# Kernel tuning notes

Measured on AMD Instinct MI355X. Metric: run time of the kernel, lower is better.

Reference implementation:

```python
import jax, jax.numpy as jnp
import numpy as np
from functools import partial

HID = 256
HOR = 5

def _lin(k, i, o):
    return jax.random.normal(k, (i, o), jnp.float32) / np.sqrt(i)

def setup_inputs() -> dict:
    key = jax.random.key(0)
    ks = jax.random.split(key, 32)
    B, T, D, Hf, Wf = 4, 16, 768, 16, 16
    H, W = 1024, 1024
    inp = {}
    inp['features'] = jax.random.normal(ks[0], (B, T, D, Hf, Wf), jnp.float32)
    inp['predictions'] = jax.random.uniform(ks[1], (B, T, 1, H, W), dtype=jnp.float32)
    # position encoder: 4 -> HID -> HID
    inp['pe_w1'] = _lin(ks[2], 4, HID); inp['pe_b1'] = jnp.zeros((HID,), jnp.float32)
    inp['pe_w2'] = _lin(ks[3], HID, HID); inp['pe_b2'] = jnp.zeros((HID,), jnp.float32)
    # 2-layer LSTM, gate order i,f,g,o (torch convention)
    inp['wih0'] = _lin(ks[4], HID, 4 * HID); inp['whh0'] = _lin(ks[5], HID, 4 * HID)
    inp['bih0'] = jnp.zeros((4 * HID,), jnp.float32); inp['bhh0'] = jnp.zeros((4 * HID,), jnp.float32)
    inp['wih1'] = _lin(ks[6], HID, 4 * HID); inp['whh1'] = _lin(ks[7], HID, 4 * HID)
    inp['bih1'] = jnp.zeros((4 * HID,), jnp.float32); inp['bhh1'] = jnp.zeros((4 * HID,), jnp.float32)
    # motion predictor: HID -> HID -> HID/2 -> HOR*4
    inp['mp_w1'] = _lin(ks[8], HID, HID); inp['mp_b1'] = jnp.zeros((HID,), jnp.float32)
    inp['mp_w2'] = _lin(ks[9], HID, HID // 2); inp['mp_b2'] = jnp.zeros((HID // 2,), jnp.float32)
    inp['mp_w3'] = _lin(ks[10], HID // 2, HOR * 4); inp['mp_b3'] = jnp.zeros((HOR * 4,), jnp.float32)
    # confidence: HID -> HID/2 -> HOR
    inp['cf_w1'] = _lin(ks[11], HID, HID // 2); inp['cf_b1'] = jnp.zeros((HID // 2,), jnp.float32)
    inp['cf_w2'] = _lin(ks[12], HID // 2, HOR); inp['cf_b2'] = jnp.zeros((HOR,), jnp.float32)
    return inp

def _extract_bboxes(predictions):
    # predictions: (B,T,1,H,W) -> bboxes (B,T,4) in (cx,cy,w,h), normalized
    B, T, _, H, W = predictions.shape
    mask = predictions[:, :, 0] > 0.5  # (B,T,H,W)
    xs = jnp.arange(W, dtype=jnp.float32)           # (W,)
    ys = jnp.arange(H, dtype=jnp.float32)[:, None]  # (H,1)
    big = jnp.float32(H + W)
    x_min = jnp.min(jnp.where(mask, xs, big), axis=(-2, -1))
    x_max = jnp.max(jnp.where(mask, xs, -1.0), axis=(-2, -1))
    y_min = jnp.min(jnp.where(mask, ys, big), axis=(-2, -1))
    y_max = jnp.max(jnp.where(mask, ys, -1.0), axis=(-2, -1))
    has = jnp.any(mask, axis=(-2, -1))  # (B,T)
    cx = (x_min + x_max) / 2.0 / W
    cy = (y_min + y_max) / 2.0 / H
    w = (x_max - x_min) / W
    h = (y_max - y_min) / H
    bbox = jnp.stack([cx, cy, w, h], axis=-1)  # (B,T,4)
    default = jnp.array([0.5, 0.5, 0.1, 0.1], dtype=jnp.float32)
    return jnp.where(has[..., None], bbox, default)

def _lstm_layer(x, wih, whh, bih, bhh):
    # x: (B,T,HID); returns (hs (B,T,H), h_final (B,H))
    B = x.shape[0]
    xg = jnp.einsum('bti,ig->btg', x, wih) + bih  # (B,T,4H)
    def step(carry, xg_t):
        h, c = carry
        g = xg_t + h @ whh + bhh
        i, f, gg, o = jnp.split(g, 4, axis=-1)
        i = jax.nn.sigmoid(i); f = jax.nn.sigmoid(f)
        gg = jnp.tanh(gg); o = jax.nn.sigmoid(o)
        c = f * c + i * gg
        h = o * jnp.tanh(c)
        return (h, c), h
    z = jnp.zeros((B, HID), x.dtype)
    (h, c), hs = jax.lax.scan(step, (z, z), xg.swapaxes(0, 1))
    return hs.swapaxes(0, 1), h

def reference(features, predictions, pe_w1, pe_b1, pe_w2, pe_b2,
              wih0, whh0, bih0, bhh0, wih1, whh1, bih1, bhh1,
              mp_w1, mp_b1, mp_w2, mp_b2, mp_w3, mp_b3,
              cf_w1, cf_b1, cf_w2, cf_b2):
    B, T = features.shape[:2]
    bboxes = _extract_bboxes(predictions)  # (B,T,4)
    pos = jax.nn.relu(bboxes @ pe_w1 + pe_b1)
    pos = jax.nn.relu(pos @ pe_w2 + pe_b2)  # (B,T,HID)
    h1, _ = _lstm_layer(pos, wih0, whh0, bih0, bhh0)
    motion_features, last_hidden = _lstm_layer(h1, wih1, whh1, bih1, bhh1)
    x = jax.nn.relu(last_hidden @ mp_w1 + mp_b1)
    x = jax.nn.relu(x @ mp_w2 + mp_b2)
    predicted_deltas = (x @ mp_w3 + mp_b3).reshape(B, HOR, 4)
    last_bbox = bboxes[:, -1:, :]
    predicted_bboxes = last_bbox + jnp.cumsum(predicted_deltas, axis=1)
    c = jax.nn.relu(last_hidden @ cf_w1 + cf_b1)
    confidence = jax.nn.sigmoid(c @ cf_w2 + cf_b2)  # (B,HOR)
    predicted_locations = predicted_bboxes[..., :2]
    predicted_scales = predicted_bboxes[..., 2:]
    return (predicted_deltas, predicted_bboxes, predicted_locations,
            predicted_scales, motion_features, confidence, bboxes)
```

## Files before the change

kernel.cpp:

```cpp
#include <hip/hip_runtime.h>
#include <math.h>

#define BIGI (1 << 30)

#define PM_OFF    0
#define MM_OFF    8192
#define POS2_OFF  8448
#define HT0_OFF   24832
#define HT2_OFF   57600
#define HT_WORDS  36864

#define OUT_DELTAS 0
#define OUT_PBB    80
#define OUT_LOC    160
#define OUT_SCL    200
#define OUT_MF     240
#define OUT_CONF   16624
#define OUT_BBOX   16644

__device__ __forceinline__ float sigmoidf_(float x) { return 1.0f / (1.0f + expf(-x)); }

__device__ __forceinline__ void storeh(unsigned long long* p, float h, int tag) {
    unsigned long long v =
        ((unsigned long long)(unsigned)tag << 32) | (unsigned long long)__float_as_uint(h);
    __hip_atomic_store(p, v, __ATOMIC_RELAXED, __HIP_MEMORY_SCOPE_AGENT);
}
__device__ __forceinline__ float pollh(const unsigned long long* p, int tag) {
    unsigned long long v = __hip_atomic_load(p, __ATOMIC_RELAXED, __HIP_MEMORY_SCOPE_AGENT);
    while ((int)(v >> 32) != tag) {
        __builtin_amdgcn_s_sleep(1);
        v = __hip_atomic_load(p, __ATOMIC_RELAXED, __HIP_MEMORY_SCOPE_AGENT);
    }
    return __uint_as_float((unsigned)v);
}

__global__ __launch_bounds__(256) void k_minmax(const float4* __restrict__ pred,
                                                int* __restrict__ pm) {
    int img = blockIdx.x >> 5;
    int chunk = blockIdx.x & 31;
    int tid = threadIdx.x;
    int base = img * 262144 + chunk * 8192 + tid;
    int xmn = BIGI, xmx = -1, ymn = BIGI, ymx = -1;
#pragma unroll 4
    for (int i = 0; i < 32; ++i) {
        int idx4 = base + i * 256;
        float4 v = pred[idx4];
        int x = (idx4 << 2) & 1023;
        int y = (idx4 >> 8) & 1023;
        bool m0 = v.x > 0.5f, m1 = v.y > 0.5f, m2 = v.z > 0.5f, m3 = v.w > 0.5f;
        int cmn = m0 ? x : (m1 ? x + 1 : (m2 ? x + 2 : (m3 ? x + 3 : BIGI)));
        int cmx = m3 ? x + 3 : (m2 ? x + 2 : (m1 ? x + 1 : (m0 ? x : -1)));
        xmn = min(xmn, cmn);
        xmx = max(xmx, cmx);
        if (m0 | m1 | m2 | m3) { ymn = min(ymn, y); ymx = max(ymx, y); }
    }
    for (int off = 32; off > 0; off >>= 1) {
        xmn = min(xmn, __shfl_down(xmn, off));
        xmx = max(xmx, __shfl_down(xmx, off));
        ymn = min(ymn, __shfl_down(ymn, off));
        ymx = max(ymx, __shfl_down(ymx, off));
    }
    __shared__ int red[4][4];
    int wave = tid >> 6;
    if ((tid & 63) == 0) { red[0][wave] = xmn; red[1][wave] = xmx; red[2][wave] = ymn; red[3][wave] = ymx; }
    __syncthreads();
    if (tid == 0) {
        xmn = min(min(red[0][0], red[0][1]), min(red[0][2], red[0][3]));
        xmx = max(max(red[1][0], red[1][1]), max(red[1][2], red[1][3]));
        ymn = min(min(red[2][0], red[2][1]), min(red[2][2], red[2][3]));
        ymx = max(max(red[3][0], red[3][1]), max(red[3][2], red[3][3]));
        ((int4*)pm)[blockIdx.x] = make_int4(xmn, xmx, ymn, ymx);
    }
}

__global__ __launch_bounds__(256) void k_prep(const int* __restrict__ pm,
    int* __restrict__ mm, int* __restrict__ ht,
    const float* __restrict__ pe_w1, const float* __restrict__ pe_b1,
    const float* __restrict__ pe_w2, const float* __restrict__ pe_b2,
    float* __restrict__ pos2, float* __restrict__ out) {
    __shared__ float bb[4];
    __shared__ float p1[256];
    int w = blockIdx.x, tid = threadIdx.x;
    for (int i = w * 256 + tid; i < HT_WORDS; i += 64 * 256) ht[i] = 0;
    if (tid < 64) {
        int xmn = BIGI, xmx = -1, ymn = BIGI, ymx = -1;
        if (tid < 32) {
            int4 v = ((const int4*)pm)[w * 32 + tid];
            xmn = v.x; xmx = v.y; ymn = v.z; ymx = v.w;
        }
        for (int off = 32; off > 0; off >>= 1) {
            xmn = min(xmn, __shfl_down(xmn, off));
            xmx = max(xmx, __shfl_down(xmx, off));
            ymn = min(ymn, __shfl_down(ymn, off));
            ymx = max(ymx, __shfl_down(ymx, off));
        }
        if (tid == 0) {
            mm[w * 4 + 0] = xmn; mm[w * 4 + 1] = xmx;
            mm[w * 4 + 2] = ymn; mm[w * 4 + 3] = ymx;
            float cx, cy, bw, bh;
            if (xmx >= 0) {
                cx = (float)(xmn + xmx) * (0.5f / 1024.0f);
                cy = (float)(ymn + ymx) * (0.5f / 1024.0f);
                bw = (float)(xmx - xmn) * (1.0f / 1024.0f);
                bh = (float)(ymx - ymn) * (1.0f / 1024.0f);
            } else { cx = 0.5f; cy = 0.5f; bw = 0.1f; bh = 0.1f; }
            bb[0] = cx; bb[1] = cy; bb[2] = bw; bb[3] = bh;
            out[OUT_BBOX + w * 4 + 0] = cx; out[OUT_BBOX + w * 4 + 1] = cy;
            out[OUT_BBOX + w * 4 + 2] = bw; out[OUT_BBOX + w * 4 + 3] = bh;
        }
    }
    __syncthreads();
    {
        float v = bb[0] * pe_w1[tid] + bb[1] * pe_w1[256 + tid] +
                  bb[2] * pe_w1[512 + tid] + bb[3] * pe_w1[768 + tid] + pe_b1[tid];
        p1[tid] = fmaxf(v, 0.0f);
    }
    __syncthreads();
    float acc = pe_b2[tid];
#pragma unroll 4
    for (int k = 0; k < 256; ++k) acc += p1[k] * pe_w2[k * 256 + tid];
    pos2[w * 256 + tid] = fmaxf(acc, 0.0f);
}

__global__ __launch_bounds__(256, 1) void k_lstm(
    const float* __restrict__ wih0, const float* __restrict__ whh0,
    const float* __restrict__ bih0, const float* __restrict__ bhh0,
    const float* __restrict__ wih1, const float* __restrict__ whh1,
    const float* __restrict__ bih1, const float* __restrict__ bhh1,
    const float* __restrict__ mp_w1, const float* __restrict__ mp_b1,
    const float* __restrict__ mp_w2, const float* __restrict__ mp_b2,
    const float* __restrict__ mp_w3, const float* __restrict__ mp_b3,
    const float* __restrict__ cf_w1, const float* __restrict__ cf_b1,
    const float* __restrict__ cf_w2, const float* __restrict__ cf_b2,
    const float* __restrict__ pos2, unsigned long long* __restrict__ hT0,
    unsigned long long* __restrict__ hT2,
    const int* __restrict__ mm, float* __restrict__ out) {
    __shared__ float px[4096];
    __shared__ float partX[4096];
    __shared__ float xgl[2048];
    __shared__ float hsm[256];
    __shared__ float part[256];
    __shared__ float gatesL[128];
    const int tid = threadIdx.x;
    const int b = blockIdx.x >> 3, g = blockIdx.x & 7;
    const int j = tid & 127, kh = tid >> 7;
    const int col = ((j >> 5) << 8) + g * 32 + (j & 31);
    float4 wreg[32];

    for (int layer = 0; layer < 2; ++layer) {
        const float* wih = layer ? wih1 : wih0;
        const float* whh = layer ? whh1 : whh0;
        const float* bih = layer ? bih1 : bih0;
        const float* bhh = layer ? bhh1 : bhh0;

        if (layer == 0) {
            for (int i = tid; i < 4096; i += 256) px[i] = pos2[b * 4096 + i];
        } else {
            for (int i = tid; i < 4096; i += 256) {
                int t = i >> 8, unit = i & 255;
                px[i] = pollh(&hT0[((b * 16 + t) << 8) + unit], t + 1);
            }
        }
#pragma unroll
        for (int k4 = 0; k4 < 32; ++k4) {
            int r = kh * 128 + k4 * 4;
            wreg[k4].x = wih[(r + 0) * 1024 + col];
            wreg[k4].y = wih[(r + 1) * 1024 + col];
            wreg[k4].z = wih[(r + 2) * 1024 + col];
            wreg[k4].w = wih[(r + 3) * 1024 + col];
        }
        __syncthreads();
        for (int t = 0; t < 16; ++t) {
            float a = 0.0f;
            const float4* p4 = (const float4*)&px[t * 256 + kh * 128];
#pragma unroll
            for (int k4 = 0; k4 < 32; ++k4) {
                float4 h4 = p4[k4];
                a += h4.x * wreg[k4].x + h4.y * wreg[k4].y + h4.z * wreg[k4].z + h4.w * wreg[k4].w;
            }
            partX[kh * 2048 + t * 128 + j] = a;
        }
        __syncthreads();
        {
            float bsum = bih[col] + bhh[col];
            int t0 = tid >> 7;
            for (int i = 0; i < 8; ++i) {
                int t = t0 + 2 * i;
                xgl[t * 128 + j] = partX[t * 128 + j] + partX[2048 + t * 128 + j] + bsum;
            }
        }
#pragma unroll
        for (int k4 = 0; k4 < 32; ++k4) {
            int r = kh * 128 + k4 * 4;
            wreg[k4].x = whh[(r + 0) * 1024 + col];
            wreg[k4].y = whh[(r + 1) * 1024 + col];
            wreg[k4].z = whh[(r + 2) * 1024 + col];
            wreg[k4].w = whh[(r + 3) * 1024 + col];
        }
        __syncthreads();

        float cst = 0.0f;
        for (int t = 0; t < 16; ++t) {
            if (t) {
                const unsigned long long* src = (layer == 0)
                    ? &hT0[((b * 16 + (t - 1)) << 8) + tid]
                    : &hT2[(((b << 1) | ((t - 1) & 1)) << 8) + tid];
                hsm[tid] = pollh(src, layer * 16 + t);
            }
            __syncthreads();
            float a = 0.0f;
            if (t) {
                const float4* h4p = (const float4*)&hsm[kh * 128];
#pragma unroll
                for (int k4 = 0; k4 < 32; ++k4) {
                    float4 h4 = h4p[k4];
                    a += h4.x * wreg[k4].x + h4.y * wreg[k4].y + h4.z * wreg[k4].z + h4.w * wreg[k4].w;
                }
            }
            part[tid] = a;
            __syncthreads();
            if (tid < 128) gatesL[tid] = part[tid] + part[128 + tid] + xgl[t * 128 + tid];
            __syncthreads();
            if (tid < 32) {
                float gi = gatesL[tid], gf = gatesL[32 + tid];
                float gg = gatesL[64 + tid], go = gatesL[96 + tid];
                float i_ = sigmoidf_(gi), f_ = sigmoidf_(gf);
                float g_ = tanhf(gg), o_ = sigmoidf_(go);
                cst = f_ * cst + i_ * g_;
                float h = o_ * tanhf(cst);
                int unit = g * 32 + tid;
                int tag = layer * 16 + t + 1;
                if (layer == 0) {
                    storeh(&hT0[((b * 16 + t) << 8) + unit], h, tag);
                } else {
                    storeh(&hT2[(((b << 1) | (t & 1)) << 8) + unit], h, tag);
                    out[OUT_MF + (b * 16 + t) * 256 + unit] = h;
                }
            }
        }
    }

    if (g != 0) return;
    __syncthreads();
    float* lh = px;
    float* x1 = px + 256;
    float* c1 = px + 512;
    float* x2 = px + 768;
    float* dl = px + 896;
    lh[tid] = pollh(&hT2[((b << 1) | 1) << 8 | tid], 32);
    __syncthreads();
    {
        float a = mp_b1[tid];
#pragma unroll 4
        for (int k = 0; k < 256; ++k) a += lh[k] * mp_w1[k * 256 + tid];
        x1[tid] = fmaxf(a, 0.0f);
    }
    if (tid < 128) {
        float a = cf_b1[tid];
#pragma unroll 4
        for (int k = 0; k < 256; ++k) a += lh[k] * cf_w1[k * 128 + tid];
        c1[tid] = fmaxf(a, 0.0f);
    }
    __syncthreads();
    if (tid < 128) {
        float a = mp_b2[tid];
#pragma unroll 4
        for (int k = 0; k < 256; ++k) a += x1[k] * mp_w2[k * 128 + tid];
        x2[tid] = fmaxf(a, 0.0f);
    } else if (tid < 133) {
        int jj = tid - 128;
        float a = cf_b2[jj];
#pragma unroll 4
        for (int k = 0; k < 128; ++k) a += c1[k] * cf_w2[k * 5 + jj];
        out[OUT_CONF + b * 5 + jj] = sigmoidf_(a);
    }
    __syncthreads();
    if (tid < 20) {
        float a = mp_b3[tid];
#pragma unroll 4
        for (int k = 0; k < 128; ++k) a += x2[k] * mp_w3[k * 20 + tid];
        dl[tid] = a;
        out[OUT_DELTAS + b * 20 + tid] = a;
    }
    __syncthreads();
    if (tid < 4) {
        int img = b * 16 + 15;
        int xmn = mm[img * 4 + 0], xmx = mm[img * 4 + 1];
        int ymn = mm[img * 4 + 2], ymx = mm[img * 4 + 3];
        float v;
        if (xmx >= 0) {
            if (tid == 0)      v = (float)(xmn + xmx) * (0.5f / 1024.0f);
            else if (tid == 1) v = (float)(ymn + ymx) * (0.5f / 1024.0f);
            else if (tid == 2) v = (float)(xmx - xmn) * (1.0f / 1024.0f);
            else               v = (float)(ymx - ymn) * (1.0f / 1024.0f);
        } else v = (tid < 2) ? 0.5f : 0.1f;
        float acc = v;
        for (int hh = 0; hh < 5; ++hh) {
            acc += dl[hh * 4 + tid];
            out[OUT_PBB + b * 20 + hh * 4 + tid] = acc;
            if (tid < 2) out[OUT_LOC + b * 10 + hh * 2 + tid] = acc;
            else out[OUT_SCL + b * 10 + hh * 2 + (tid - 2)] = acc;
        }
    }
}

extern "C" void kernel_launch(void* const* d_in, const int* in_sizes, int n_in,
                              void* d_out, int out_size, void* d_ws, size_t ws_size,
                              hipStream_t stream) {
    (void)in_sizes; (void)n_in; (void)out_size; (void)ws_size;
    const float* pred = (const float*)d_in[1];
    const float* pe_w1 = (const float*)d_in[2];
    const float* pe_b1 = (const float*)d_in[3];
    const float* pe_w2 = (const float*)d_in[4];
    const float* pe_b2 = (const float*)d_in[5];
    const float* wih0 = (const float*)d_in[6];
    const float* whh0 = (const float*)d_in[7];
    const float* bih0 = (const float*)d_in[8];
    const float* bhh0 = (const float*)d_in[9];
    const float* wih1 = (const float*)d_in[10];
    const float* whh1 = (const float*)d_in[11];
    const float* bih1 = (const float*)d_in[12];
    const float* bhh1 = (const float*)d_in[13];
    const float* mp_w1 = (const float*)d_in[14];
    const float* mp_b1 = (const float*)d_in[15];
    const float* mp_w2 = (const float*)d_in[16];
    const float* mp_b2 = (const float*)d_in[17];
    const float* mp_w3 = (const float*)d_in[18];
    const float* mp_b3 = (const float*)d_in[19];
    const float* cf_w1 = (const float*)d_in[20];
    const float* cf_b1 = (const float*)d_in[21];
    const float* cf_w2 = (const float*)d_in[22];
    const float* cf_b2 = (const float*)d_in[23];
    float* out = (float*)d_out;
    int* wsi = (int*)d_ws;
    float* wsf = (float*)d_ws;

    hipLaunchKernelGGL(k_minmax, dim3(64 * 32), dim3(256), 0, stream,
                       (const float4*)pred, wsi + PM_OFF);
    hipLaunchKernelGGL(k_prep, dim3(64), dim3(256), 0, stream,
                       wsi + PM_OFF, wsi + MM_OFF, wsi + HT0_OFF,
                       pe_w1, pe_b1, pe_w2, pe_b2,
                       wsf + POS2_OFF, out);
    hipLaunchKernelGGL(k_lstm, dim3(32), dim3(256), 0, stream,
                       wih0, whh0, bih0, bhh0,
                       wih1, whh1, bih1, bhh1,
                       mp_w1, mp_b1, mp_w2, mp_b2, mp_w3, mp_b3,
                       cf_w1, cf_b1, cf_w2, cf_b2,
                       wsf + POS2_OFF,
                       (unsigned long long*)(wsi + HT0_OFF),
                       (unsigned long long*)(wsi + HT2_OFF),
                       wsi + MM_OFF, out);
}
```

Before: 658.2 us.

## Fuse prep into LSTM kernel and pipeline both layers concurrently across blocks

```diff
diff --git a/kernel.cpp b/kernel.cpp
--- a/kernel.cpp
+++ b/kernel.cpp
@@ -4,11 +4,11 @@
 #define BIGI (1 << 30)
 
 #define PM_OFF    0
-#define MM_OFF    8192
-#define POS2_OFF  8448
-#define HT0_OFF   24832
-#define HT2_OFF   57600
-#define HT_WORDS  36864
+#define HT0_OFF   8192
+#define HT2_OFF   40960
+#define DONE_OFF  45056
+#define ZERO_BEG  8192
+#define ZERO_END  45057
 
 #define OUT_DELTAS 0
 #define OUT_PBB    80
@@ -35,10 +35,12 @@
 }
 
 __global__ __launch_bounds__(256) void k_minmax(const float4* __restrict__ pred,
-                                                int* __restrict__ pm) {
+                                                int* __restrict__ ws) {
+    int tid = threadIdx.x;
+    for (int i = ZERO_BEG + blockIdx.x * 256 + tid; i < ZERO_END; i += 2048 * 256)
+        ws[i] = 0;
     int img = blockIdx.x >> 5;
     int chunk = blockIdx.x & 31;
-    int tid = threadIdx.x;
     int base = img * 262144 + chunk * 8192 + tid;
     int xmn = BIGI, xmx = -1, ymn = BIGI, ymx = -1;
 #pragma unroll 4
@@ -69,60 +71,23 @@
         xmx = max(max(red[1][0], red[1][1]), max(red[1][2], red[1][3]));
         ymn = min(min(red[2][0], red[2][1]), min(red[2][2], red[2][3]));
         ymx = max(max(red[3][0], red[3][1]), max(red[3][2], red[3][3]));
-        ((int4*)pm)[blockIdx.x] = make_int4(xmn, xmx, ymn, ymx);
-    }
-}
-
-__global__ __launch_bounds__(256) void k_prep(const int* __restrict__ pm,
-    int* __restrict__ mm, int* __restrict__ ht,
+        ((int4*)(ws + PM_OFF))[blockIdx.x] = make_int4(xmn, xmx, ymn, ymx);
+    }
+}
+
+__device__ __forceinline__ void mk_bbox(int xmn, int xmx, int ymn, int ymx,
+                                        float* o) {
+    if (xmx >= 0) {
+        o[0] = (float)(xmn + xmx) * (0.5f / 1024.0f);
+        o[1] = (float)(ymn + ymx) * (0.5f / 1024.0f);
+        o[2] = (float)(xmx - xmn) * (1.0f / 1024.0f);
+        o[3] = (float)(ymx - ymn) * (1.0f / 1024.0f);
+    } else { o[0] = 0.5f; o[1] = 0.5f; o[2] = 0.1f; o[3] = 0.1f; }
+}
+
+__global__ __launch_bounds__(256, 1) void k_fused(
     const float* __restrict__ pe_w1, const float* __restrict__ pe_b1,
     const float* __restrict__ pe_w2, const float* __restrict__ pe_b2,
-    float* __restrict__ pos2, float* __restrict__ out) {
-    __shared__ float bb[4];
-    __shared__ float p1[256];
-    int w = blockIdx.x, tid = threadIdx.x;
-    for (int i = w * 256 + tid; i < HT_WORDS; i += 64 * 256) ht[i] = 0;
-    if (tid < 64) {
-        int xmn = BIGI, xmx = -1, ymn = BIGI, ymx = -1;
-        if (tid < 32) {
-            int4 v = ((const int4*)pm)[w * 32 + tid];
-            xmn = v.x; xmx = v.y; ymn = v.z; ymx = v.w;
-        }
-        for (int off = 32; off > 0; off >>= 1) {
-            xmn = min(xmn, __shfl_down(xmn, off));
-            xmx = max(xmx, __shfl_down(xmx, off));
-            ymn = min(ymn, __shfl_down(ymn, off));
-            ymx = max(ymx, __shfl_down(ymx, off));
-        }
-        if (tid == 0) {
-            mm[w * 4 + 0] = xmn; mm[w * 4 + 1] = xmx;
-            mm[w * 4 + 2] = ymn; mm[w * 4 + 3] = ymx;
-            float cx, cy, bw, bh;
-            if (xmx >= 0) {
-                cx = (float)(xmn + xmx) * (0.5f / 1024.0f);
-                cy = (float)(ymn + ymx) * (0.5f / 1024.0f);
-                bw = (float)(xmx - xmn) * (1.0f / 1024.0f);
-                bh = (float)(ymx - ymn) * (1.0f / 1024.0f);
-            } else { cx = 0.5f; cy = 0.5f; bw = 0.1f; bh = 0.1f; }
-            bb[0] = cx; bb[1] = cy; bb[2] = bw; bb[3] = bh;
-            out[OUT_BBOX + w * 4 + 0] = cx; out[OUT_BBOX + w * 4 + 1] = cy;
-            out[OUT_BBOX + w * 4 + 2] = bw; out[OUT_BBOX + w * 4 + 3] = bh;
-        }
-    }
-    __syncthreads();
-    {
-        float v = bb[0] * pe_w1[tid] + bb[1] * pe_w1[256 + tid] +
-                  bb[2] * pe_w1[512 + tid] + bb[3] * pe_w1[768 + tid] + pe_b1[tid];
-        p1[tid] = fmaxf(v, 0.0f);
-    }
-    __syncthreads();
-    float acc = pe_b2[tid];
-#pragma unroll 4
-    for (int k = 0; k < 256; ++k) acc += p1[k] * pe_w2[k * 256 + tid];
-    pos2[w * 256 + tid] = fmaxf(acc, 0.0f);
-}
-
-__global__ __launch_bounds__(256, 1) void k_lstm(
     const float* __restrict__ wih0, const float* __restrict__ whh0,
     const float* __restrict__ bih0, const float* __restrict__ bhh0,
     const float* __restrict__ wih1, const float* __restrict__ whh1,
@@ -132,122 +97,197 @@
     const float* __restrict__ mp_w3, const float* __restrict__ mp_b3,
     const float* __restrict__ cf_w1, const float* __restrict__ cf_b1,
     const float* __restrict__ cf_w2, const float* __restrict__ cf_b2,
-    const float* __restrict__ pos2, unsigned long long* __restrict__ hT0,
-    unsigned long long* __restrict__ hT2,
-    const int* __restrict__ mm, float* __restrict__ out) {
-    __shared__ float px[4096];
-    __shared__ float partX[4096];
-    __shared__ float xgl[2048];
+    const int4* __restrict__ pm4, unsigned long long* __restrict__ hT0,
+    unsigned long long* __restrict__ hT2, int* __restrict__ done,
+    float* __restrict__ out) {
+    __shared__ float sPX[4096];
+    __shared__ float sP1[4096];
+    __shared__ float sBB[64];
     __shared__ float hsm[256];
+    __shared__ float h2sm[256];
     __shared__ float part[256];
-    __shared__ float gatesL[128];
-    const int tid = threadIdx.x;
-    const int b = blockIdx.x >> 3, g = blockIdx.x & 7;
+    const int tid = threadIdx.x, blk = blockIdx.x;
+
+    if (blk >= 64) {
+        float a0 = 0.f, a1 = 1.f, a2 = 2.f, a3 = 3.f, a4 = 4.f, a5 = 5.f, a6 = 6.f, a7 = 7.f;
+        const float m = 1.0000001f, c = 0.9999999f;
+        for (;;) {
+#pragma unroll
+            for (int i = 0; i < 128; ++i) {
+                a0 = fmaf(a0, m, c); a1 = fmaf(a1, m, c); a2 = fmaf(a2, m, c); a3 = fmaf(a3, m, c);
+                a4 = fmaf(a4, m, c); a5 = fmaf(a5, m, c); a6 = fmaf(a6, m, c); a7 = fmaf(a7, m, c);
+            }
+            if (__hip_atomic_load(done, __ATOMIC_RELAXED, __HIP_MEMORY_SCOPE_AGENT) >= 4) break;
+        }
+        asm volatile("" :: "v"(a0), "v"(a1), "v"(a2), "v"(a3), "v"(a4), "v"(a5), "v"(a6), "v"(a7));
+        return;
+    }
+
+    const int layer = blk >> 5;
+    const int b = (blk >> 3) & 3, g = blk & 7;
     const int j = tid & 127, kh = tid >> 7;
     const int col = ((j >> 5) << 8) + g * 32 + (j & 31);
-    float4 wreg[32];
-
-    for (int layer = 0; layer < 2; ++layer) {
-        const float* wih = layer ? wih1 : wih0;
-        const float* whh = layer ? whh1 : whh0;
-        const float* bih = layer ? bih1 : bih0;
-        const float* bhh = layer ? bhh1 : bhh0;
-
+
+    if (layer == 0) {
+        {
+            int il = tid >> 4, c2 = (tid & 15) * 2;
+            int4 A = pm4[(b * 16 + il) * 32 + c2];
+            int4 B = pm4[(b * 16 + il) * 32 + c2 + 1];
+            int xmn = min(A.x, B.x), xmx = max(A.y, B.y);
+            int ymn = min(A.z, B.z), ymx = max(A.w, B.w);
+            for (int off = 8; off > 0; off >>= 1) {
+                xmn = min(xmn, __shfl_down(xmn, off, 16));
+                xmx = max(xmx, __shfl_down(xmx, off, 16));
+                ymn = min(ymn, __shfl_down(ymn, off, 16));
+                ymx = max(ymx, __shfl_down(ymx, off, 16));
+            }
+            if ((tid & 15) == 0) {
+                float bb[4];
+                mk_bbox(xmn, xmx, ymn, ymx, bb);
+                sBB[il * 4 + 0] = bb[0]; sBB[il * 4 + 1] = bb[1];
+                sBB[il * 4 + 2] = bb[2]; sBB[il * 4 + 3] = bb[3];
+                if (g == 0) {
+                    out[OUT_BBOX + (b * 16 + il) * 4 + 0] = bb[0];
+                    out[OUT_BBOX + (b * 16 + il) * 4 + 1] = bb[1];
+                    out[OUT_BBOX + (b * 16 + il) * 4 + 2] = bb[2];
+                    out[OUT_BBOX + (b * 16 + il) * 4 + 3] = bb[3];
+                }
+            }
+        }
+        __syncthreads();
+        {
+            float w0 = pe_w1[tid], w1 = pe_w1[256 + tid];
+            float w2 = pe_w1[512 + tid], w3 = pe_w1[768 + tid], b1v = pe_b1[tid];
+#pragma unroll
+            for (int i = 0; i < 16; ++i) {
+                float v = sBB[i * 4] * w0 + sBB[i * 4 + 1] * w1 +
+                          sBB[i * 4 + 2] * w2 + sBB[i * 4 + 3] * w3 + b1v;
+                sP1[i * 256 + tid] = fmaxf(v, 0.0f);
+            }
+        }
+        __syncthreads();
+        {
+            float acc[16];
+            float b2v = pe_b2[tid];
+#pragma unroll
+            for (int i = 0; i < 16; ++i) acc[i] = b2v;
+            for (int k = 0; k < 256; ++k) {
+                float wv = pe_w2[k * 256 + tid];
+#pragma unroll
+                for (int i = 0; i < 16; ++i) acc[i] += sP1[i * 256 + k] * wv;
+            }
+#pragma unroll
+            for (int i = 0; i < 16; ++i) sPX[i * 256 + tid] = fmaxf(acc[i], 0.0f);
+        }
+        __syncthreads();
+    }
+
+    const float* wih = layer ? wih1 : wih0;
+    const float* whh = layer ? whh1 : whh0;
+    const float* bih = layer ? bih1 : bih0;
+    const float* bhh = layer ? bhh1 : bhh0;
+    float4 wi[32], wh[32];
+#pragma unroll
+    for (int k4 = 0; k4 < 32; ++k4) {
+        int r = kh * 128 + k4 * 4;
+        wi[k4].x = wih[(r + 0) * 1024 + col];
+        wi[k4].y = wih[(r + 1) * 1024 + col];
+        wi[k4].z = wih[(r + 2) * 1024 + col];
+        wi[k4].w = wih[(r + 3) * 1024 + col];
+        wh[k4].x = whh[(r + 0) * 1024 + col];
+        wh[k4].y = whh[(r + 1) * 1024 + col];
+        wh[k4].z = whh[(r + 2) * 1024 + col];
+        wh[k4].w = whh[(r + 3) * 1024 + col];
+    }
+    float bs0 = 0.f, bs1 = 0.f, bs2 = 0.f, bs3 = 0.f;
+    if (tid < 32) {
+        int u = g * 32 + tid;
+        bs0 = bih[u] + bhh[u];
+        bs1 = bih[256 + u] + bhh[256 + u];
+        bs2 = bih[512 + u] + bhh[512 + u];
+        bs3 = bih[768 + u] + bhh[768 + u];
+    }
+
+    float cst = 0.0f;
+    for (int t = 0; t < 16; ++t) {
         if (layer == 0) {
-            for (int i = tid; i < 4096; i += 256) px[i] = pos2[b * 4096 + i];
+            if (t) hsm[tid] = pollh(&hT0[((b * 16 + t - 1) << 8) + tid], t);
         } else {
-            for (int i = tid; i < 4096; i += 256) {
-                int t = i >> 8, unit = i & 255;
-                px[i] = pollh(&hT0[((b * 16 + t) << 8) + unit], t + 1);
-            }
-        }
-#pragma unroll
-        for (int k4 = 0; k4 < 32; ++k4) {
-            int r = kh * 128 + k4 * 4;
-            wreg[k4].x = wih[(r + 0) * 1024 + col];
-            wreg[k4].y = wih[(r + 1) * 1024 + col];
-            wreg[k4].z = wih[(r + 2) * 1024 + col];
-            wreg[k4].w = wih[(r + 3) * 1024 + col];
-        }
-        __syncthreads();
-        for (int t = 0; t < 16; ++t) {
-            float a = 0.0f;
-            const float4* p4 = (const float4*)&px[t * 256 + kh * 128];
-#pragma unroll
-            for (int k4 = 0; k4 < 32; ++k4) {
-                float4 h4 = p4[k4];
-                a += h4.x * wreg[k4].x + h4.y * wreg[k4].y + h4.z * wreg[k4].z + h4.w * wreg[k4].w;
-            }
-            partX[kh * 2048 + t * 128 + j] = a;
-        }
-        __syncthreads();
-        {
-            float bsum = bih[col] + bhh[col];
-            int t0 = tid >> 7;
-            for (int i = 0; i < 8; ++i) {
-                int t = t0 + 2 * i;
-                xgl[t * 128 + j] = partX[t * 128 + j] + partX[2048 + t * 128 + j] + bsum;
-            }
-        }
-#pragma unroll
-        for (int k4 = 0; k4 < 32; ++k4) {
-            int r = kh * 128 + k4 * 4;
-            wreg[k4].x = whh[(r + 0) * 1024 + col];
-            wreg[k4].y = whh[(r + 1) * 1024 + col];
-            wreg[k4].z = whh[(r + 2) * 1024 + col];
-            wreg[k4].w = whh[(r + 3) * 1024 + col];
-        }
-        __syncthreads();
-
-        float cst = 0.0f;
-        for (int t = 0; t < 16; ++t) {
+            hsm[tid] = pollh(&hT0[((b * 16 + t) << 8) + tid], t + 1);
+            if (t) h2sm[tid] = pollh(&hT2[(((b << 1) | ((t - 1) & 1)) << 8) + tid], t);
+        }
+        __syncthreads();
+        float a = 0.0f;
+        if (layer == 0) {
+            const float4* xr = (const float4*)&sPX[t * 256 + kh * 128];
+#pragma unroll
+            for (int k = 0; k < 32; ++k) {
+                float4 x = xr[k];
+                a += x.x * wi[k].x + x.y * wi[k].y + x.z * wi[k].z + x.w * wi[k].w;
+            }
             if (t) {
-                const unsigned long long* src = (layer == 0)
-                    ? &hT0[((b * 16 + (t - 1)) << 8) + tid]
-                    : &hT2[(((b << 1) | ((t - 1) & 1)) << 8) + tid];
-                hsm[tid] = pollh(src, layer * 16 + t);
-            }
-            __syncthreads();
-            float a = 0.0f;
+                const float4* hr = (const float4*)&hsm[kh * 128];
+#pragma unroll
+                for (int k = 0; k < 32; ++k) {
+                    float4 h = hr[k];
+                    a += h.x * wh[k].x + h.y * wh[k].y + h.z * wh[k].z + h.w * wh[k].w;
+                }
+            }
+        } else {
+            const float4* xr = (const float4*)&hsm[kh * 128];
+#pragma unroll
+            for (int k = 0; k < 32; ++k) {
+                float4 x = xr[k];
+                a += x.x * wi[k].x + x.y * wi[k].y + x.z * wi[k].z + x.w * wi[k].w;
+            }
             if (t) {
-                const float4* h4p = (const float4*)&hsm[kh * 128];
-#pragma unroll
-                for (int k4 = 0; k4 < 32; ++k4) {
-                    float4 h4 = h4p[k4];
-                    a += h4.x * wreg[k4].x + h4.y * wreg[k4].y + h4.z * wreg[k4].z + h4.w * wreg[k4].w;
+                const float4* hr = (const float4*)&h2sm[kh * 128];
+#pragma unroll
+                for (int k = 0; k < 32; ++k) {
+                    float4 h = hr[k];
+                    a += h.x * wh[k].x + h.y * wh[k].y + h.z * wh[k].z + h.w * wh[k].w;
                 }
             }
-            part[tid] = a;
-            __syncthreads();
-            if (tid < 128) gatesL[tid] = part[tid] + part[128 + tid] + xgl[t * 128 + tid];
-            __syncthreads();
-            if (tid < 32) {
-                float gi = gatesL[tid], gf = gatesL[32 + tid];
-                float gg = gatesL[64 + tid], go = gatesL[96 + tid];
-                float i_ = sigmoidf_(gi), f_ = sigmoidf_(gf);
-                float g_ = tanhf(gg), o_ = sigmoidf_(go);
-                cst = f_ * cst + i_ * g_;
-                float h = o_ * tanhf(cst);
-                int unit = g * 32 + tid;
-                int tag = layer * 16 + t + 1;
-                if (layer == 0) {
-                    storeh(&hT0[((b * 16 + t) << 8) + unit], h, tag);
-                } else {
-                    storeh(&hT2[(((b << 1) | (t & 1)) << 8) + unit], h, tag);
-                    out[OUT_MF + (b * 16 + t) * 256 + unit] = h;
-                }
-            }
-        }
-    }
-
-    if (g != 0) return;
-    __syncthreads();
-    float* lh = px;
-    float* x1 = px + 256;
-    float* c1 = px + 512;
-    float* x2 = px + 768;
-    float* dl = px + 896;
-    lh[tid] = pollh(&hT2[((b << 1) | 1) << 8 | tid], 32);
+        }
+        part[tid] = a;
+        __syncthreads();
+        if (tid < 32) {
+            float gi = part[tid] + part[128 + tid] + bs0;
+            float gf = part[32 + tid] + part[160 + tid] + bs1;
+            float gg = part[64 + tid] + part[192 + tid] + bs2;
+            float go = part[96 + tid] + part[224 + tid] + bs3;
+            float i_ = sigmoidf_(gi), f_ = sigmoidf_(gf);
+            float g_ = tanhf(gg), o_ = sigmoidf_(go);
+            cst = f_ * cst + i_ * g_;
+            float h = o_ * tanhf(cst);
+            int unit = g * 32 + tid;
+            if (layer == 0) {
+                storeh(&hT0[((b * 16 + t) << 8) + unit], h, t + 1);
+            } else {
+                storeh(&hT2[(((b << 1) | (t & 1)) << 8) + unit], h, t + 1);
+                out[OUT_MF + (b * 16 + t) * 256 + unit] = h;
+            }
+        }
+    }
+    if (layer == 0 || g != 0) return;
+
+    float* lh = sPX;
+    float* x1 = sPX + 256;
+    float* c1 = sPX + 512;
+    float* x2 = sPX + 640;
+    float* dl = sPX + 768;
+    lh[tid] = pollh(&hT2[(((b << 1) | 1) << 8) + tid], 16);
+    if (tid < 32) {
+        int4 v = pm4[(b * 16 + 15) * 32 + tid];
+        int xmn = v.x, xmx = v.y, ymn = v.z, ymx = v.w;
+        for (int off = 16; off > 0; off >>= 1) {
+            xmn = min(xmn, __shfl_down(xmn, off, 32));
+            xmx = max(xmx, __shfl_down(xmx, off, 32));
+            ymn = min(ymn, __shfl_down(ymn, off, 32));
+            ymx = max(ymx, __shfl_down(ymx, off, 32));
+        }
+        if (tid == 0) mk_bbox(xmn, xmx, ymn, ymx, sBB);
+    }
     __syncthreads();
     {
         float a = mp_b1[tid];
@@ -284,17 +324,7 @@
     }
     __syncthreads();
     if (tid < 4) {
-        int img = b * 16 + 15;
-        int xmn = mm[img * 4 + 0], xmx = mm[img * 4 + 1];
-        int ymn = mm[img * 4 + 2], ymx = mm[img * 4 + 3];
-        float v;
-        if (xmx >= 0) {
-            if (tid == 0)      v = (float)(xmn + xmx) * (0.5f / 1024.0f);
-            else if (tid == 1) v = (float)(ymn + ymx) * (0.5f / 1024.0f);
-            else if (tid == 2) v = (float)(xmx - xmn) * (1.0f / 1024.0f);
-            else               v = (float)(ymx - ymn) * (1.0f / 1024.0f);
-        } else v = (tid < 2) ? 0.5f : 0.1f;
-        float acc = v;
+        float acc = sBB[tid];
         for (int hh = 0; hh < 5; ++hh) {
             acc += dl[hh * 4 + tid];
             out[OUT_PBB + b * 20 + hh * 4 + tid] = acc;
@@ -302,6 +332,8 @@
             else out[OUT_SCL + b * 10 + hh * 2 + (tid - 2)] = acc;
         }
     }
+    __syncthreads();
+    if (tid == 0) atomicAdd(done, 1);
 }
 
 extern "C" void kernel_launch(void* const* d_in, const int* in_sizes, int n_in,
@@ -333,21 +365,17 @@
     const float* cf_b2 = (const float*)d_in[23];
     float* out = (float*)d_out;
     int* wsi = (int*)d_ws;
-    float* wsf = (float*)d_ws;
 
     hipLaunchKernelGGL(k_minmax, dim3(64 * 32), dim3(256), 0, stream,
-                       (const float4*)pred, wsi + PM_OFF);
-    hipLaunchKernelGGL(k_prep, dim3(64), dim3(256), 0, stream,
-                       wsi + PM_OFF, wsi + MM_OFF, wsi + HT0_OFF,
+                       (const float4*)pred, wsi);
+    hipLaunchKernelGGL(k_fused, dim3(192), dim3(256), 0, stream,
                        pe_w1, pe_b1, pe_w2, pe_b2,
-                       wsf + POS2_OFF, out);
-    hipLaunchKernelGGL(k_lstm, dim3(32), dim3(256), 0, stream,
                        wih0, whh0, bih0, bhh0,
                        wih1, whh1, bih1, bhh1,
                        mp_w1, mp_b1, mp_w2, mp_b2, mp_w3, mp_b3,
                        cf_w1, cf_b1, cf_w2, cf_b2,
-                       wsf + POS2_OFF,
+                       (const int4*)(wsi + PM_OFF),
                        (unsigned long long*)(wsi + HT0_OFF),
                        (unsigned long long*)(wsi + HT2_OFF),
-                       wsi + MM_OFF, out);
-}
+                       wsi + DONE_OFF, out);
+}
```

After: 603.6 us. 1.09x faster.
